# Performance work log

Hardware: AMD Instinct MI355X
Metric: run time of the kernel (lower is better)

The kernel has to match this reference:

```python
import jax, jax.numpy as jnp
import numpy as np

B, T, IN, H, OUT, L = 1024, 128, 32, 256, 32, 3  # batch, times, input_dim, hidden_dim, output_dim, num_layers
STEP = 0.05  # odeint rk4 step_size; times grid is aligned to it


def lipswish(x):
    return 0.909 * x * jax.nn.sigmoid(x)


def setup_inputs() -> dict:
    key = jax.random.key(0)
    ks = jax.random.split(key, 4)
    coeffs = jax.random.normal(ks[0], (B, T, IN), dtype=jnp.float32)
    times = jnp.arange(T, dtype=jnp.float32) * STEP
    # learned parameters
    W_init = jax.random.normal(ks[1], (IN, H), dtype=jnp.float32) * (1.0 / np.sqrt(IN))
    b_init = jnp.zeros((H,), dtype=jnp.float32)
    # vector field f: L lipswish hidden layers + final linear, all H->H
    Wf = jax.random.normal(ks[2], (L + 1, H, H), dtype=jnp.float32) * (1.0 / np.sqrt(H))
    bf = jnp.zeros((L + 1, H), dtype=jnp.float32)
    Wd = jax.random.normal(ks[3], (H, OUT), dtype=jnp.float32) * (1.0 / np.sqrt(H))
    bd = jnp.zeros((OUT,), dtype=jnp.float32)
    return dict(coeffs=coeffs, times=times, W_init=W_init, b_init=b_init,
                Wf=Wf, bf=bf, Wd=Wd, bd=bd)


def reference(coeffs, times, W_init, b_init, Wf, bf, Wd, bd):
    # vector field func.f(t, y): autonomous MLP (inject_noise=False, so g unused)
    def f(y):
        h = y
        for i in range(L):
            h = lipswish(h @ Wf[i] + bf[i])
        return h @ Wf[L] + bf[L]

    # y0 = initial(X.evaluate(times))[:, 0, :] -> only the first time point seeds the state
    y0 = coeffs[:, 0, :] @ W_init + b_init  # [B, H]

    dts = times[1:] - times[:-1]  # each interval = one RK4 step (grid aligned to step_size)

    def step(y, dt):
        k1 = f(y)
        k2 = f(y + 0.5 * dt * k1)
        k3 = f(y + 0.5 * dt * k2)
        k4 = f(y + dt * k3)
        y_next = y + (dt / 6.0) * (k1 + 2.0 * k2 + 2.0 * k3 + k4)
        return y_next, y_next

    _, ys = jax.lax.scan(step, y0, dts)  # [T-1, B, H]
    z = jnp.concatenate([y0[None], ys], axis=0)  # [T, B, H]
    z = jnp.transpose(z, (1, 0, 2))  # [B, T, H]
    return z @ Wd + bd  # [B, T, OUT]
```

## Files before the change

### kernel.cpp

```cpp
#include <hip/hip_runtime.h>


#define T_ 128
#define IN_ 32
#define H_ 256

typedef _Float16 half8 __attribute__((ext_vector_type(8)));
typedef _Float16 half4 __attribute__((ext_vector_type(4)));
typedef float f32x4 __attribute__((ext_vector_type(4)));

__device__ __forceinline__ f32x4 mfma16(half8 a, half8 b, f32x4 c) {
    return __builtin_amdgcn_mfma_f32_16x16x32_f16(a, b, c, 0, 0, 0);
}

__device__ __forceinline__ half4 cvt4(f32x4 v) {
    half4 h;
    h[0] = (_Float16)v[0]; h[1] = (_Float16)v[1];
    h[2] = (_Float16)v[2]; h[3] = (_Float16)v[3];
    return h;
}

__device__ __forceinline__ f32x4 lips4(f32x4 v) {
    f32x4 r;
#pragma unroll
    for (int e = 0; e < 4; ++e) {
        float x = v[e];
        r[e] = 0.909f * x / (1.f + __expf(-x));
    }
    return r;
}

#define RDH(BUFB, KS) (*(const half8*)(ht + (BUFB) + hb2 + (((KS)*64) ^ sswz)))
#define RDA(C, KS)    (*(const half8*)(w0b + (C)*8192 + (KS)*1024))

#define STORE_TILE(BUFB, V0, V1) do {                 \
    *(half4*)(ht + (BUFB) + wo0)        = cvt4(V0);   \
    *(half4*)(ht + (BUFB) + (wo0 ^ 32)) = cvt4(V1);   \
} while (0)

#define LAYER_REG(LYI, BUFB) do {                      \
    half8 b0 = RDH(BUFB, 0), b1 = RDH(BUFB, 1);        \
    acc0 = mfma16(wreg[LYI][0][0], b0, acc0);          \
    acc1 = mfma16(wreg[LYI][1][0], b0, acc1);          \
    b0 = RDH(BUFB, 2);                                 \
    acc0 = mfma16(wreg[LYI][0][1], b1, acc0);          \
    acc1 = mfma16(wreg[LYI][1][1], b1, acc1);          \
    b1 = RDH(BUFB, 3);                                 \
    acc0 = mfma16(wreg[LYI][0][2], b0, acc0);          \
    acc1 = mfma16(wreg[LYI][1][2], b0, acc1);          \
    b0 = RDH(BUFB, 4);                                 \
    acc0 = mfma16(wreg[LYI][0][3], b1, acc0);          \
    acc1 = mfma16(wreg[LYI][1][3], b1, acc1);          \
    b1 = RDH(BUFB, 5);                                 \
    acc0 = mfma16(wreg[LYI][0][4], b0, acc0);          \
    acc1 = mfma16(wreg[LYI][1][4], b0, acc1);          \
    b0 = RDH(BUFB, 6);                                 \
    acc0 = mfma16(wreg[LYI][0][5], b1, acc0);          \
    acc1 = mfma16(wreg[LYI][1][5], b1, acc1);          \
    b1 = RDH(BUFB, 7);                                 \
    acc0 = mfma16(wreg[LYI][0][6], b0, acc0);          \
    acc1 = mfma16(wreg[LYI][1][6], b0, acc1);          \
    acc0 = mfma16(wreg[LYI][0][7], b1, acc0);          \
    acc1 = mfma16(wreg[LYI][1][7], b1, acc1);          \
} while (0)

#define LAYER_L0(BUFB) do {                                    \
    half8 b0 = RDH(BUFB, 0), b1 = RDH(BUFB, 1);                \
    half8 x0 = RDA(0, 0), z0 = RDA(1, 0);                      \
    half8 x1 = RDA(0, 1), z1 = RDA(1, 1);                      \
    acc0 = mfma16(x0, b0, acc0); acc1 = mfma16(z0, b0, acc1);  \
    b0 = RDH(BUFB, 2); x0 = RDA(0, 2); z0 = RDA(1, 2);         \
    acc0 = mfma16(x1, b1, acc0); acc1 = mfma16(z1, b1, acc1);  \
    b1 = RDH(BUFB, 3); x1 = RDA(0, 3); z1 = RDA(1, 3);         \
    acc0 = mfma16(x0, b0, acc0); acc1 = mfma16(z0, b0, acc1);  \
    b0 = RDH(BUFB, 4); x0 = RDA(0, 4); z0 = RDA(1, 4);         \
    acc0 = mfma16(x1, b1, acc0); acc1 = mfma16(z1, b1, acc1);  \
    b1 = RDH(BUFB, 5); x1 = RDA(0, 5); z1 = RDA(1, 5);         \
    acc0 = mfma16(x0, b0, acc0); acc1 = mfma16(z0, b0, acc1);  \
    b0 = RDH(BUFB, 6); x0 = RDA(0, 6); z0 = RDA(1, 6);         \
    acc0 = mfma16(x1, b1, acc0); acc1 = mfma16(z1, b1, acc1);  \
    b1 = RDH(BUFB, 7); x1 = RDA(0, 7); z1 = RDA(1, 7);         \
    acc0 = mfma16(x0, b0, acc0); acc1 = mfma16(z0, b0, acc1);  \
    acc0 = mfma16(x1, b1, acc0); acc1 = mfma16(z1, b1, acc1);  \
} while (0)

#define ACT_STORE(LY, BUFB) do {                                          \
    f32x4 bia0 = *(const f32x4*)(bias + (LY)*H_ + w*32 + lk*4);           \
    f32x4 bia1 = *(const f32x4*)(bias + (LY)*H_ + w*32 + 16 + lk*4);      \
    f32x4 v0 = lips4(acc0 + bia0);                                        \
    f32x4 v1 = lips4(acc1 + bia1);                                        \
    STORE_TILE(BUFB, v0, v1);                                             \
    __syncthreads();                                                      \
} while (0)

__global__ __launch_bounds__(512)
__attribute__((amdgpu_waves_per_eu(2, 2)))
void ncde_kernel(const float* __restrict__ coeffs,
                 const float* __restrict__ times,
                 const float* __restrict__ W_init,
                 const float* __restrict__ b_init,
                 const float* __restrict__ Wf,
                 const float* __restrict__ bfv,
                 _Float16* __restrict__ ybuf)
{
    extern __shared__ char smem[];
    _Float16* w0   = (_Float16*)smem;
    char*     ht   = smem + 131072;
    float*    bias = (float*)(smem + 131072 + 16384);

    const int tid = threadIdx.x;
    const int l   = tid & 63;
    const int w   = tid >> 6;
    const int lr  = l & 15;
    const int lk  = l >> 4;
    const int bc  = blockIdx.x;
    const int swz = (lr & 7) << 4;

    const int hb2  = lr*512 + ((lk*16) ^ (swz & 48));
    const int sswz = swz & 64;
    const int wo0  = lr*512 + (((w*64) | (lk*8)) ^ swz);
    const char* w0b = (const char*)w0 + (size_t)(2*w)*8192 + l*16;

    for (int i = tid; i < 4*H_; i += 512) bias[i] = bfv[i];

    for (int e = tid; e < 8192; e += 512) {
        int mt = e >> 9, ks = (e >> 6) & 7, ln = e & 63;
        int colh = mt*16 + (ln & 15);
        int row0 = ks*32 + ((ln >> 4) << 3);
        const float* src = Wf + (size_t)row0 * H_ + colh;
        half8 v;
#pragma unroll
        for (int j = 0; j < 8; ++j) v[j] = (_Float16)src[(size_t)j * H_];
        *(half8*)(w0 + (size_t)e * 8) = v;
    }

    half8 wreg[3][2][8];
#pragma unroll
    for (int ly = 0; ly < 3; ++ly)
#pragma unroll
        for (int c = 0; c < 2; ++c)
#pragma unroll
            for (int ks = 0; ks < 8; ++ks) {
                const float* src = Wf + ((size_t)(ly + 1) * H_ + ks*32 + lk*8) * H_
                                      + w*32 + c*16 + lr;
                half8 v;
#pragma unroll
                for (int j = 0; j < 8; ++j) v[j] = (_Float16)src[(size_t)j * H_];
                wreg[ly][c][ks] = v;
            }

    f32x4 y0v, y1v;
    {
        const float* crow = coeffs + (size_t)(bc*16 + lr) * (T_ * IN_);
#pragma unroll
        for (int c = 0; c < 2; ++c) {
            f32x4 acc;
#pragma unroll
            for (int r = 0; r < 4; ++r) {
                int hcol = w*32 + c*16 + lk*4 + r;
                float s = b_init[hcol];
                for (int k = 0; k < IN_; ++k)
                    s += crow[k] * W_init[(size_t)k * H_ + hcol];
                acc[r] = s;
            }
            if (c == 0) y0v = acc; else y1v = acc;
        }
    }

    STORE_TILE(0, y0v, y1v);
    __syncthreads();
    {
        int drow = tid >> 5, dcb = (tid & 31) << 4;
        uint4 vv = *(const uint4*)(ht + drow*512 + (dcb ^ ((drow & 7) << 4)));
        *(uint4*)((char*)ybuf + ((size_t)(bc*T_) << 13) + tid*16) = vv;
    }

#pragma unroll 1
    for (int st = 0; st < T_ - 1; ++st) {
        float dt = times[st + 1] - times[st];
        f32x4 ks0, ks1;
#pragma unroll 1
        for (int s = 0; s < 4; ++s) {
            f32x4 acc0 = f32x4{0.f,0.f,0.f,0.f}, acc1 = f32x4{0.f,0.f,0.f,0.f};
            LAYER_L0(0);
            ACT_STORE(0, 8192);
            acc0 = f32x4{0.f,0.f,0.f,0.f};  acc1 = f32x4{0.f,0.f,0.f,0.f};
            LAYER_REG(0, 8192);
            ACT_STORE(1, 0);
            acc0 = f32x4{0.f,0.f,0.f,0.f};  acc1 = f32x4{0.f,0.f,0.f,0.f};
            LAYER_REG(1, 0);
            ACT_STORE(2, 8192);
            acc0 = f32x4{0.f,0.f,0.f,0.f};  acc1 = f32x4{0.f,0.f,0.f,0.f};
            LAYER_REG(2, 8192);
            f32x4 k0, k1;
            {
                f32x4 bia0 = *(const f32x4*)(bias + 3*H_ + w*32 + lk*4);
                f32x4 bia1 = *(const f32x4*)(bias + 3*H_ + w*32 + 16 + lk*4);
                k0 = acc0 + bia0; k1 = acc1 + bia1;
            }
            if (s == 0)     { ks0 = k0;       ks1 = k1; }
            else if (s < 3) { ks0 += 2.f*k0;  ks1 += 2.f*k1; }
            else            { ks0 += k0;      ks1 += k1; }
            if (s < 3) {
                float cy = (s == 2) ? dt : 0.5f*dt;
                f32x4 yn0 = y0v + cy*k0, yn1 = y1v + cy*k1;
                STORE_TILE(0, yn0, yn1);
            } else {
                float c6 = dt * (1.f/6.f);
                y0v += c6*ks0; y1v += c6*ks1;
                STORE_TILE(0, y0v, y1v);
            }
            __syncthreads();
        }
        {
            int drow = tid >> 5, dcb = (tid & 31) << 4;
            uint4 vv = *(const uint4*)(ht + drow*512 + (dcb ^ ((drow & 7) << 4)));
            *(uint4*)((char*)ybuf + ((size_t)(bc*T_ + st + 1) << 13) + tid*16) = vv;
        }
    }
}

__global__ __launch_bounds__(64)
void proj_kernel(const _Float16* __restrict__ ybuf,
                 const float* __restrict__ Wd,
                 const float* __restrict__ bd,
                 float* __restrict__ out)
{
    const int l  = threadIdx.x;
    const int lr = l & 15, lk = l >> 4;
    const int bc = blockIdx.x;
    const int tg = blockIdx.y;

    half8 wd[2][8];
#pragma unroll
    for (int c = 0; c < 2; ++c)
#pragma unroll
        for (int ks = 0; ks < 8; ++ks) {
            const float* src = Wd + (size_t)(ks*32 + lk*8) * 32 + c*16 + lr;
            half8 v;
#pragma unroll
            for (int j = 0; j < 8; ++j) v[j] = (_Float16)src[(size_t)j * 32];
            wd[c][ks] = v;
        }
    f32x4 bd0 = *(const f32x4*)(bd + lk*4);
    f32x4 bd1 = *(const f32x4*)(bd + 16 + lk*4);

    for (int t = tg*16; t < tg*16 + 16; ++t) {
        const _Float16* yt = ybuf + ((size_t)(bc*T_) + t) * 4096;
        f32x4 a0 = f32x4{0.f,0.f,0.f,0.f}, a1 = f32x4{0.f,0.f,0.f,0.f};
#pragma unroll
        for (int ks = 0; ks < 8; ++ks) {
            half8 b = *(const half8*)(yt + lr*256 + ks*32 + lk*8);
            a0 = mfma16(wd[0][ks], b, a0);
            a1 = mfma16(wd[1][ks], b, a1);
        }
        float* op = out + ((size_t)(bc*16 + lr) * T_ + t) * 32;
        *(f32x4*)(op + lk*4)      = a0 + bd0;
        *(f32x4*)(op + 16 + lk*4) = a1 + bd1;
    }
}

extern "C" void kernel_launch(void* const* d_in, const int* in_sizes, int n_in,
                              void* d_out, int out_size, void* d_ws, size_t ws_size,
                              hipStream_t stream) {
    const float* coeffs = (const float*)d_in[0];
    const float* times  = (const float*)d_in[1];
    const float* W_init = (const float*)d_in[2];
    const float* b_init = (const float*)d_in[3];
    const float* Wf     = (const float*)d_in[4];
    const float* bfv    = (const float*)d_in[5];
    const float* Wd     = (const float*)d_in[6];
    const float* bd     = (const float*)d_in[7];
    _Float16* ybuf = (_Float16*)d_ws;
    float* out = (float*)d_out;

    const size_t lds_bytes = 131072 + 16384 + 4096;
    hipLaunchKernelGGL(ncde_kernel, dim3(64), dim3(512), lds_bytes, stream,
                       coeffs, times, W_init, b_init, Wf, bfv, ybuf);
    hipLaunchKernelGGL(proj_kernel, dim3(64, 8), dim3(64), 0, stream,
                       ybuf, Wd, bd, out);
}
```

Baseline: 1.934 ms.

## Halve workgroup to 4 waves, each owning 64 output columns with register weights

The ODE kernel now runs 256 threads (4 waves) per block instead of 8 waves, and each wave computes four 16-column tiles instead of two. Layers 1-3 therefore hold 96 half8 weight registers per lane, with waves_per_eu set to 1. Each hidden-state fragment read from LDS now feeds four MFMAs instead of two. The bias is folded into the accumulator initialization, and the LDS read addressing is simplified. The aim is to cut LDS traffic and the cost of the barriers between the serial layers, at the risk of register pressure or spills and fewer waves per CU to hide latency.

```diff
diff --git a/kernel.cpp b/kernel.cpp
--- a/kernel.cpp
+++ b/kernel.cpp
@@ -30,71 +30,69 @@
     return r;
 }
 
-#define RDH(BUFB, KS) (*(const half8*)(ht + (BUFB) + hb2 + (((KS)*64) ^ sswz)))
-#define RDA(C, KS)    (*(const half8*)(w0b + (C)*8192 + (KS)*1024))
-
-#define STORE_TILE(BUFB, V0, V1) do {                 \
-    *(half4*)(ht + (BUFB) + wo0)        = cvt4(V0);   \
-    *(half4*)(ht + (BUFB) + (wo0 ^ 32)) = cvt4(V1);   \
-} while (0)
-
-#define LAYER_REG(LYI, BUFB) do {                      \
-    half8 b0 = RDH(BUFB, 0), b1 = RDH(BUFB, 1);        \
-    acc0 = mfma16(wreg[LYI][0][0], b0, acc0);          \
-    acc1 = mfma16(wreg[LYI][1][0], b0, acc1);          \
-    b0 = RDH(BUFB, 2);                                 \
-    acc0 = mfma16(wreg[LYI][0][1], b1, acc0);          \
-    acc1 = mfma16(wreg[LYI][1][1], b1, acc1);          \
-    b1 = RDH(BUFB, 3);                                 \
-    acc0 = mfma16(wreg[LYI][0][2], b0, acc0);          \
-    acc1 = mfma16(wreg[LYI][1][2], b0, acc1);          \
-    b0 = RDH(BUFB, 4);                                 \
-    acc0 = mfma16(wreg[LYI][0][3], b1, acc0);          \
-    acc1 = mfma16(wreg[LYI][1][3], b1, acc1);          \
-    b1 = RDH(BUFB, 5);                                 \
-    acc0 = mfma16(wreg[LYI][0][4], b0, acc0);          \
-    acc1 = mfma16(wreg[LYI][1][4], b0, acc1);          \
-    b0 = RDH(BUFB, 6);                                 \
-    acc0 = mfma16(wreg[LYI][0][5], b1, acc0);          \
-    acc1 = mfma16(wreg[LYI][1][5], b1, acc1);          \
-    b1 = RDH(BUFB, 7);                                 \
-    acc0 = mfma16(wreg[LYI][0][6], b0, acc0);          \
-    acc1 = mfma16(wreg[LYI][1][6], b0, acc1);          \
-    acc0 = mfma16(wreg[LYI][0][7], b1, acc0);          \
-    acc1 = mfma16(wreg[LYI][1][7], b1, acc1);          \
-} while (0)
-
-#define LAYER_L0(BUFB) do {                                    \
-    half8 b0 = RDH(BUFB, 0), b1 = RDH(BUFB, 1);                \
-    half8 x0 = RDA(0, 0), z0 = RDA(1, 0);                      \
-    half8 x1 = RDA(0, 1), z1 = RDA(1, 1);                      \
-    acc0 = mfma16(x0, b0, acc0); acc1 = mfma16(z0, b0, acc1);  \
-    b0 = RDH(BUFB, 2); x0 = RDA(0, 2); z0 = RDA(1, 2);         \
-    acc0 = mfma16(x1, b1, acc0); acc1 = mfma16(z1, b1, acc1);  \
-    b1 = RDH(BUFB, 3); x1 = RDA(0, 3); z1 = RDA(1, 3);         \
-    acc0 = mfma16(x0, b0, acc0); acc1 = mfma16(z0, b0, acc1);  \
-    b0 = RDH(BUFB, 4); x0 = RDA(0, 4); z0 = RDA(1, 4);         \
-    acc0 = mfma16(x1, b1, acc0); acc1 = mfma16(z1, b1, acc1);  \
-    b1 = RDH(BUFB, 5); x1 = RDA(0, 5); z1 = RDA(1, 5);         \
-    acc0 = mfma16(x0, b0, acc0); acc1 = mfma16(z0, b0, acc1);  \
-    b0 = RDH(BUFB, 6); x0 = RDA(0, 6); z0 = RDA(1, 6);         \
-    acc0 = mfma16(x1, b1, acc0); acc1 = mfma16(z1, b1, acc1);  \
-    b1 = RDH(BUFB, 7); x1 = RDA(0, 7); z1 = RDA(1, 7);         \
-    acc0 = mfma16(x0, b0, acc0); acc1 = mfma16(z0, b0, acc1);  \
-    acc0 = mfma16(x1, b1, acc0); acc1 = mfma16(z1, b1, acc1);  \
-} while (0)
-
-#define ACT_STORE(LY, BUFB) do {                                          \
-    f32x4 bia0 = *(const f32x4*)(bias + (LY)*H_ + w*32 + lk*4);           \
-    f32x4 bia1 = *(const f32x4*)(bias + (LY)*H_ + w*32 + 16 + lk*4);      \
-    f32x4 v0 = lips4(acc0 + bia0);                                        \
-    f32x4 v1 = lips4(acc1 + bia1);                                        \
-    STORE_TILE(BUFB, v0, v1);                                             \
-    __syncthreads();                                                      \
-} while (0)
-
-__global__ __launch_bounds__(512)
-__attribute__((amdgpu_waves_per_eu(2, 2)))
+#define RDH(KS, BUF) (*(const half8*)(ht + (BUF) + (((KS) & 1) ? (po + ((KS)-1)*64) : (pe + (KS)*64))))
+#define RDA(C, KS)   (*(const half8*)(w0b + (C)*8192 + (KS)*1024))
+
+#define KSTEP(LYI, KS, BREG) \
+    acc0 = mfma16(wreg[LYI][0][KS], BREG, acc0); \
+    acc1 = mfma16(wreg[LYI][1][KS], BREG, acc1); \
+    acc2 = mfma16(wreg[LYI][2][KS], BREG, acc2); \
+    acc3 = mfma16(wreg[LYI][3][KS], BREG, acc3);
+
+#define LAYER_REG(LYI, BUF) do {                    \
+    half8 b0 = RDH(0, BUF), b1 = RDH(1, BUF);       \
+    KSTEP(LYI, 0, b0) b0 = RDH(2, BUF);             \
+    KSTEP(LYI, 1, b1) b1 = RDH(3, BUF);             \
+    KSTEP(LYI, 2, b0) b0 = RDH(4, BUF);             \
+    KSTEP(LYI, 3, b1) b1 = RDH(5, BUF);             \
+    KSTEP(LYI, 4, b0) b0 = RDH(6, BUF);             \
+    KSTEP(LYI, 5, b1) b1 = RDH(7, BUF);             \
+    KSTEP(LYI, 6, b0)                               \
+    KSTEP(LYI, 7, b1)                               \
+} while (0)
+
+#define KSTEP0(KS, BREG) {                              \
+    half8 x;                                            \
+    x = RDA(0, KS); acc0 = mfma16(x, BREG, acc0);       \
+    x = RDA(1, KS); acc1 = mfma16(x, BREG, acc1);       \
+    x = RDA(2, KS); acc2 = mfma16(x, BREG, acc2);       \
+    x = RDA(3, KS); acc3 = mfma16(x, BREG, acc3); }
+
+#define LAYER_L0(BUF) do {                          \
+    half8 b0 = RDH(0, BUF), b1 = RDH(1, BUF);       \
+    KSTEP0(0, b0) b0 = RDH(2, BUF);                 \
+    KSTEP0(1, b1) b1 = RDH(3, BUF);                 \
+    KSTEP0(2, b0) b0 = RDH(4, BUF);                 \
+    KSTEP0(3, b1) b1 = RDH(5, BUF);                 \
+    KSTEP0(4, b0) b0 = RDH(6, BUF);                 \
+    KSTEP0(5, b1) b1 = RDH(7, BUF);                 \
+    KSTEP0(6, b0)                                   \
+    KSTEP0(7, b1)                                   \
+} while (0)
+
+#define ACC_INIT(LY) do {                                       \
+    acc0 = *(const f32x4*)(biasb + (LY)*1024 + 0);              \
+    acc1 = *(const f32x4*)(biasb + (LY)*1024 + 64);             \
+    acc2 = *(const f32x4*)(biasb + (LY)*1024 + 128);            \
+    acc3 = *(const f32x4*)(biasb + (LY)*1024 + 192);            \
+} while (0)
+
+#define ACT_STORE(BUF) do {                                     \
+    *(half4*)(ht + (BUF) + wo0) = cvt4(lips4(acc0));            \
+    *(half4*)(ht + (BUF) + wo1) = cvt4(lips4(acc1));            \
+    *(half4*)(ht + (BUF) + wo2) = cvt4(lips4(acc2));            \
+    *(half4*)(ht + (BUF) + wo3) = cvt4(lips4(acc3));            \
+    __syncthreads();                                            \
+} while (0)
+
+#define STORE_Y(BUF, V0, V1, V2, V3) do {                       \
+    *(half4*)(ht + (BUF) + wo0) = cvt4(V0);                     \
+    *(half4*)(ht + (BUF) + wo1) = cvt4(V1);                     \
+    *(half4*)(ht + (BUF) + wo2) = cvt4(V2);                     \
+    *(half4*)(ht + (BUF) + wo3) = cvt4(V3);                     \
+} while (0)
+
+__global__ __attribute__((amdgpu_flat_work_group_size(256, 256), amdgpu_waves_per_eu(1, 1)))
 void ncde_kernel(const float* __restrict__ coeffs,
                  const float* __restrict__ times,
                  const float* __restrict__ W_init,
@@ -116,106 +114,101 @@
     const int bc  = blockIdx.x;
     const int swz = (lr & 7) << 4;
 
-    const int hb2  = lr*512 + ((lk*16) ^ (swz & 48));
-    const int sswz = swz & 64;
-    const int wo0  = lr*512 + (((w*64) | (lk*8)) ^ swz);
-    const char* w0b = (const char*)w0 + (size_t)(2*w)*8192 + l*16;
-
-    for (int i = tid; i < 4*H_; i += 512) bias[i] = bfv[i];
-
-    for (int e = tid; e < 8192; e += 512) {
-        int mt = e >> 9, ks = (e >> 6) & 7, ln = e & 63;
-        int colh = mt*16 + (ln & 15);
-        int row0 = ks*32 + ((ln >> 4) << 3);
-        const float* src = Wf + (size_t)row0 * H_ + colh;
+    const int hb2 = lr*512 + ((lk*16) ^ (swz & 48));
+    const int pe  = hb2 + (swz & 64);
+    const int po  = hb2 + 64 - (swz & 64);
+    const int wo_base = lr*512 + (((w*128) | (lk*8)) ^ swz);
+    const int wo0 = wo_base, wo1 = wo_base ^ 32, wo2 = wo_base ^ 64, wo3 = wo_base ^ 96;
+    const char* w0b   = (const char*)w0 + (size_t)w * 32768 + l * 16;
+    const char* biasb = (const char*)bias + w * 256 + lk * 16;
+
+    for (int i = tid; i < 4 * H_; i += 256) bias[i] = bfv[i];
+
+    for (int e = tid; e < 8192; e += 256) {
+        int ct = e >> 9, ks = (e >> 6) & 7, ln = e & 63;
+        const float* src = Wf + (size_t)(ks*32 + ((ln >> 4) << 3)) * H_ + ct*16 + (ln & 15);
         half8 v;
 #pragma unroll
         for (int j = 0; j < 8; ++j) v[j] = (_Float16)src[(size_t)j * H_];
         *(half8*)(w0 + (size_t)e * 8) = v;
     }
 
-    half8 wreg[3][2][8];
+    half8 wreg[3][4][8];
 #pragma unroll
     for (int ly = 0; ly < 3; ++ly)
 #pragma unroll
-        for (int c = 0; c < 2; ++c)
+        for (int c = 0; c < 4; ++c)
 #pragma unroll
             for (int ks = 0; ks < 8; ++ks) {
                 const float* src = Wf + ((size_t)(ly + 1) * H_ + ks*32 + lk*8) * H_
-                                      + w*32 + c*16 + lr;
+                                      + w*64 + c*16 + lr;
                 half8 v;
 #pragma unroll
                 for (int j = 0; j < 8; ++j) v[j] = (_Float16)src[(size_t)j * H_];
                 wreg[ly][c][ks] = v;
             }
 
-    f32x4 y0v, y1v;
+    f32x4 y0v, y1v, y2v, y3v;
     {
         const float* crow = coeffs + (size_t)(bc*16 + lr) * (T_ * IN_);
 #pragma unroll
-        for (int c = 0; c < 2; ++c) {
+        for (int c = 0; c < 4; ++c) {
             f32x4 acc;
 #pragma unroll
             for (int r = 0; r < 4; ++r) {
-                int hcol = w*32 + c*16 + lk*4 + r;
-                float s = b_init[hcol];
+                int col = w*64 + c*16 + lk*4 + r;
+                float s = b_init[col];
                 for (int k = 0; k < IN_; ++k)
-                    s += crow[k] * W_init[(size_t)k * H_ + hcol];
+                    s += crow[k] * W_init[(size_t)k * H_ + col];
                 acc[r] = s;
             }
-            if (c == 0) y0v = acc; else y1v = acc;
-        }
-    }
-
-    STORE_TILE(0, y0v, y1v);
+            if (c == 0) y0v = acc; else if (c == 1) y1v = acc;
+            else if (c == 2) y2v = acc; else y3v = acc;
+        }
+    }
+
+    STORE_Y(0, y0v, y1v, y2v, y3v);
     __syncthreads();
     {
-        int drow = tid >> 5, dcb = (tid & 31) << 4;
-        uint4 vv = *(const uint4*)(ht + drow*512 + (dcb ^ ((drow & 7) << 4)));
-        *(uint4*)((char*)ybuf + ((size_t)(bc*T_) << 13) + tid*16) = vv;
+        int drow = tid >> 4, dcb = (tid & 15) * 32, sw = (drow & 7) << 4;
+        const char* srcp = ht + drow * 512;
+        uint4 a = *(const uint4*)(srcp + (dcb ^ sw));
+        uint4 b = *(const uint4*)(srcp + ((dcb + 16) ^ sw));
+        char* dst = (char*)ybuf + ((size_t)(bc * T_)) * 8192 + tid * 32;
+        *(uint4*)dst = a; *(uint4*)(dst + 16) = b;
     }
 
 #pragma unroll 1
     for (int st = 0; st < T_ - 1; ++st) {
         float dt = times[st + 1] - times[st];
-        f32x4 ks0, ks1;
+        f32x4 ks0, ks1, ks2, ks3;
 #pragma unroll 1
         for (int s = 0; s < 4; ++s) {
-            f32x4 acc0 = f32x4{0.f,0.f,0.f,0.f}, acc1 = f32x4{0.f,0.f,0.f,0.f};
-            LAYER_L0(0);
-            ACT_STORE(0, 8192);
-            acc0 = f32x4{0.f,0.f,0.f,0.f};  acc1 = f32x4{0.f,0.f,0.f,0.f};
-            LAYER_REG(0, 8192);
-            ACT_STORE(1, 0);
-            acc0 = f32x4{0.f,0.f,0.f,0.f};  acc1 = f32x4{0.f,0.f,0.f,0.f};
-            LAYER_REG(1, 0);
-            ACT_STORE(2, 8192);
-            acc0 = f32x4{0.f,0.f,0.f,0.f};  acc1 = f32x4{0.f,0.f,0.f,0.f};
-            LAYER_REG(2, 8192);
-            f32x4 k0, k1;
-            {
-                f32x4 bia0 = *(const f32x4*)(bias + 3*H_ + w*32 + lk*4);
-                f32x4 bia1 = *(const f32x4*)(bias + 3*H_ + w*32 + 16 + lk*4);
-                k0 = acc0 + bia0; k1 = acc1 + bia1;
-            }
-            if (s == 0)     { ks0 = k0;       ks1 = k1; }
-            else if (s < 3) { ks0 += 2.f*k0;  ks1 += 2.f*k1; }
-            else            { ks0 += k0;      ks1 += k1; }
+            f32x4 acc0, acc1, acc2, acc3;
+            ACC_INIT(0); LAYER_L0(0);        ACT_STORE(8192);
+            ACC_INIT(1); LAYER_REG(0, 8192); ACT_STORE(0);
+            ACC_INIT(2); LAYER_REG(1, 0);    ACT_STORE(8192);
+            ACC_INIT(3); LAYER_REG(2, 8192);
+            if (s == 0)      { ks0 = acc0;        ks1 = acc1;        ks2 = acc2;        ks3 = acc3; }
+            else if (s < 3)  { ks0 += 2.f*acc0;   ks1 += 2.f*acc1;   ks2 += 2.f*acc2;   ks3 += 2.f*acc3; }
+            else             { ks0 += acc0;       ks1 += acc1;       ks2 += acc2;       ks3 += acc3; }
             if (s < 3) {
-                float cy = (s == 2) ? dt : 0.5f*dt;
-                f32x4 yn0 = y0v + cy*k0, yn1 = y1v + cy*k1;
-                STORE_TILE(0, yn0, yn1);
+                float cy = (s == 2) ? dt : 0.5f * dt;
+                STORE_Y(0, y0v + cy*acc0, y1v + cy*acc1, y2v + cy*acc2, y3v + cy*acc3);
             } else {
-                float c6 = dt * (1.f/6.f);
-                y0v += c6*ks0; y1v += c6*ks1;
-                STORE_TILE(0, y0v, y1v);
+                float c6 = dt * (1.f / 6.f);
+                y0v += c6*ks0; y1v += c6*ks1; y2v += c6*ks2; y3v += c6*ks3;
+                STORE_Y(0, y0v, y1v, y2v, y3v);
             }
             __syncthreads();
         }
         {
-            int drow = tid >> 5, dcb = (tid & 31) << 4;
-            uint4 vv = *(const uint4*)(ht + drow*512 + (dcb ^ ((drow & 7) << 4)));
-            *(uint4*)((char*)ybuf + ((size_t)(bc*T_ + st + 1) << 13) + tid*16) = vv;
+            int drow = tid >> 4, dcb = (tid & 15) * 32, sw = (drow & 7) << 4;
+            const char* srcp = ht + drow * 512;
+            uint4 a = *(const uint4*)(srcp + (dcb ^ sw));
+            uint4 b = *(const uint4*)(srcp + ((dcb + 16) ^ sw));
+            char* dst = (char*)ybuf + ((size_t)(bc * T_ + st + 1)) * 8192 + tid * 32;
+            *(uint4*)dst = a; *(uint4*)(dst + 16) = b;
         }
     }
 }
@@ -275,7 +268,7 @@
     float* out = (float*)d_out;
 
     const size_t lds_bytes = 131072 + 16384 + 4096;
-    hipLaunchKernelGGL(ncde_kernel, dim3(64), dim3(512), lds_bytes, stream,
+    hipLaunchKernelGGL(ncde_kernel, dim3(64), dim3(256), lds_bytes, stream,
                        coeffs, times, W_init, b_init, Wf, bfv, ybuf);
     hipLaunchKernelGGL(proj_kernel, dim3(64, 8), dim3(64), 0, stream,
                        ybuf, Wd, bd, out);
```

Result: slower. 2.305 ms (+19.2%).
